# Kernel tuning notes

Hardware: AMD Instinct MI355X
Metric: run time of the kernel (lower is better)

## Reference

```python
import jax, jax.numpy as jnp
import numpy as np

H = 1024      # hidden_size
I = 4096      # intermediate_size (4*H SwiGLU)
E = 8         # num_experts
TOPK = 2      # num_experts_per_tok


def setup_inputs() -> dict:
    key = jax.random.key(0)
    ks = jax.random.split(key, 6)
    B, S = 4, 2048
    hidden_states = jax.random.normal(ks[0], (B, S, H), dtype=jnp.float32)
    # router gate (no bias)
    gate_w = jax.random.normal(ks[1], (H, E), dtype=jnp.float32) * (1.0 / np.sqrt(H))
    # per-expert SwiGLU weights (xavier-ish scale)
    W1 = jax.random.normal(ks[2], (E, H, I), dtype=jnp.float32) * np.sqrt(2.0 / (H + I))
    W3 = jax.random.normal(ks[3], (E, H, I), dtype=jnp.float32) * np.sqrt(2.0 / (H + I))
    W2 = jax.random.normal(ks[4], (E, I, H), dtype=jnp.float32) * np.sqrt(2.0 / (H + I))
    # per-expert domain embedding (added to expert input), init std 0.02
    dom = jax.random.normal(ks[5], (E, H), dtype=jnp.float32) * 0.02
    return {"hidden_states": hidden_states, "gate_w": gate_w,
            "W1": W1, "W2": W2, "W3": W3, "dom": dom}


def reference(hidden_states, gate_w, W1, W2, W3, dom):
    B, S, Hd = hidden_states.shape
    x = hidden_states.reshape(-1, Hd)                      # [T, H]
    router_logits = x @ gate_w                             # [T, E]
    top_logits, top_idx = jax.lax.top_k(router_logits, TOPK)
    weights = jax.nn.softmax(top_logits, axis=-1)          # [T, K]
    # dense per-(token, expert) combine weight; 0 for unselected experts
    w_dense = jnp.einsum('tk,tke->te', weights,
                         jax.nn.one_hot(top_idx, E, dtype=weights.dtype))  # [T, E]
    out = jnp.zeros_like(x)
    for e in range(E):  # small fixed expert loop (structurally distinct weights)
        xe = x + dom[e]                                    # domain embedding add
        h = jax.nn.silu(xe @ W1[e]) * (xe @ W3[e])         # SwiGLU [T, I]
        out = out + w_dense[:, e:e + 1] * (h @ W2[e])      # weighted combine
    return out.reshape(B, S, Hd)
```

## Files before the change

kernel.cpp:

```cpp
#include <hip/hip_runtime.h>
#include <hip/hip_bf16.h>
#include <stdint.h>

#define T_TOK 8192
#define H_DIM 1024
#define I_DIM 4096
#define NEXP  8
#define BM    128
#define FBK   64
#define RT_TILES 136
#define RMAX (RT_TILES * BM)

typedef __attribute__((ext_vector_type(8))) short bf16x8;
typedef __attribute__((ext_vector_type(4))) float f32x4;

__device__ __forceinline__ unsigned short f2bf(float f) {
    unsigned int u = __float_as_uint(f);
    return (unsigned short)((u + 0x7FFFu + ((u >> 16) & 1u)) >> 16);
}
__device__ __forceinline__ unsigned int pk2(float a, float b) {
    return (unsigned int)f2bf(a) | ((unsigned int)f2bf(b) << 16);
}
__device__ __forceinline__ void gl_lds16(const void* g, void* l) {
    __builtin_amdgcn_global_load_lds(
        (const __attribute__((address_space(1))) unsigned int*)g,
        (__attribute__((address_space(3))) unsigned int*)l, 16, 0, 0);
}

__global__ __launch_bounds__(256) void router_k(const float* __restrict__ x,
                                                const float* __restrict__ gw,
                                                int2* __restrict__ ridx,
                                                float2* __restrict__ rw) {
    __shared__ float gwT[NEXP][H_DIM + 8];
    for (int i = threadIdx.x; i < H_DIM * NEXP; i += 256) {
        const int k = i >> 3, e = i & 7;
        gwT[e][k] = gw[i];
    }
    __syncthreads();
    const int wid = threadIdx.x >> 6, lane = threadIdx.x & 63;
    const int t = blockIdx.x * 4 + wid;
    const float4* xr = (const float4*)(x + (size_t)t * H_DIM);
    float acc[NEXP];
#pragma unroll
    for (int e = 0; e < NEXP; ++e) acc[e] = 0.f;
#pragma unroll
    for (int jj = 0; jj < 4; ++jj) {
        const float4 v = xr[jj * 64 + lane];
        const int kb = jj * 256 + lane * 4;
#pragma unroll
        for (int e = 0; e < NEXP; ++e) {
            const float4 g = *(const float4*)&gwT[e][kb];
            acc[e] += v.x * g.x + v.y * g.y + v.z * g.z + v.w * g.w;
        }
    }
#pragma unroll
    for (int e = 0; e < NEXP; ++e) {
#pragma unroll
        for (int off = 32; off > 0; off >>= 1) acc[e] += __shfl_xor(acc[e], off, 64);
    }
    if (lane == 0) {
        int i0 = 0; float l0 = acc[0];
#pragma unroll
        for (int e = 1; e < NEXP; ++e) if (acc[e] > l0) { l0 = acc[e]; i0 = e; }
        int i1 = -1; float l1 = -3.4e38f;
#pragma unroll
        for (int e = 0; e < NEXP; ++e) if (e != i0 && acc[e] > l1) { l1 = acc[e]; i1 = e; }
        float ee = __expf(l1 - l0);
        float w0 = 1.f / (1.f + ee);
        float w1 = 1.f - w0;
        ridx[t] = make_int2(i0, i1);
        rw[t]   = make_float2(w0, w1);
    }
}

__global__ __launch_bounds__(256) void plan_k(const int2* __restrict__ ridx,
                                              int* __restrict__ offs,
                                              int* __restrict__ rpos) {
    __shared__ int cnt[256][NEXP];
    __shared__ int base_sh[256][NEXP];
    __shared__ int tot_sh[NEXP];
    __shared__ int offs_sh[NEXP + 1];
    const int tid = threadIdx.x;
    const int t0 = tid * (T_TOK / 256);
    int c[NEXP];
#pragma unroll
    for (int e = 0; e < NEXP; ++e) c[e] = 0;
    for (int j = 0; j < T_TOK / 256; ++j) {
        const int2 ii = ridx[t0 + j];
#pragma unroll
        for (int e = 0; e < NEXP; ++e)
            c[e] += (ii.x == e ? 1 : 0) + (ii.y == e ? 1 : 0);
    }
#pragma unroll
    for (int e = 0; e < NEXP; ++e) cnt[tid][e] = c[e];
    __syncthreads();
    if (tid < NEXP) {
        int s = 0;
        for (int i = 0; i < 256; ++i) s += cnt[i][tid];
        tot_sh[tid] = s;
    }
    __syncthreads();
    if (tid == 0) {
        int o = 0;
#pragma unroll
        for (int e = 0; e < NEXP; ++e) {
            offs_sh[e] = o; offs[e] = o;
            o += (tot_sh[e] + BM - 1) & ~(BM - 1);
        }
        offs_sh[NEXP] = o; offs[NEXP] = o;
    }
    __syncthreads();
    if (tid < NEXP) {
        int run = offs_sh[tid];
        for (int i = 0; i < 256; ++i) {
            base_sh[i][tid] = run;
            run += cnt[i][tid];
        }
    }
    __syncthreads();
    int b[NEXP];
#pragma unroll
    for (int e = 0; e < NEXP; ++e) b[e] = base_sh[tid][e];
    for (int j = 0; j < T_TOK / 256; ++j) {
        const int2 ii = ridx[t0 + j];
        int r0 = 0, r1 = 0;
#pragma unroll
        for (int e = 0; e < NEXP; ++e) r0 += (ii.x == e ? b[e] : 0);
#pragma unroll
        for (int e = 0; e < NEXP; ++e) b[e] += (ii.x == e ? 1 : 0);
#pragma unroll
        for (int e = 0; e < NEXP; ++e) r1 += (ii.y == e ? b[e] : 0);
#pragma unroll
        for (int e = 0; e < NEXP; ++e) b[e] += (ii.y == e ? 1 : 0);
        rpos[2 * (t0 + j)]     = r0;
        rpos[2 * (t0 + j) + 1] = r1;
    }
}

__global__ __launch_bounds__(256) void scatter_w13t_k(
        const float* __restrict__ x, const float* __restrict__ dom,
        const int2* __restrict__ ridx, const float2* __restrict__ rw,
        const int* __restrict__ rpos, float* __restrict__ rwgt,
        unsigned short* __restrict__ xg,
        const float* __restrict__ W1, const float* __restrict__ W3,
        unsigned short* __restrict__ w13) {
    __shared__ float st[64 * 65];
    if (blockIdx.x < 2048) {
        const int wid = threadIdx.x >> 6, lane = threadIdx.x & 63;
        const int t = blockIdx.x * 4 + wid;
        const int2 ii = ridx[t];
        const float2 ww = rw[t];
        const int r0 = rpos[2 * t], r1 = rpos[2 * t + 1];
        if (lane == 0) {
            rwgt[r0] = ww.x;
            rwgt[r1] = ww.y;
        }
        const float4* xr = (const float4*)(x + (size_t)t * H_DIM);
        float4 xv[4];
#pragma unroll
        for (int jj = 0; jj < 4; ++jj) xv[jj] = xr[jj * 64 + lane];
#pragma unroll
        for (int s = 0; s < 2; ++s) {
            const int e = s ? ii.y : ii.x;
            const int rr = s ? r1 : r0;
            const float4* dr = (const float4*)(dom + (size_t)e * H_DIM);
            unsigned short* op = xg + (size_t)rr * H_DIM;
#pragma unroll
            for (int jj = 0; jj < 4; ++jj) {
                const float4 b = dr[jj * 64 + lane];
                const int kb = jj * 256 + lane * 4;
                *(uint2*)(op + kb) = make_uint2(pk2(xv[jj].x + b.x, xv[jj].y + b.y),
                                                pk2(xv[jj].z + b.z, xv[jj].w + b.w));
            }
        }
    } else {
        const int idx = blockIdx.x - 2048;
        const int nt = idx & 63;
        const int kt = (idx >> 6) & 15;
        const int z  = idx >> 10;
        const int e = z >> 1, sel = z & 1;
        const float* src = (sel ? W3 : W1) + (size_t)e * H_DIM * I_DIM;
        const int t = threadIdx.x;
        const int kr = t >> 2, c0 = (t & 3) << 4;
        const float* sp = src + (size_t)(kt * 64 + kr) * I_DIM + nt * 64 + c0;
#pragma unroll
        for (int j = 0; j < 4; ++j) {
            float4 v = *(const float4*)(sp + j * 4);
            st[kr * 65 + c0 + j*4 + 0] = v.x; st[kr * 65 + c0 + j*4 + 1] = v.y;
            st[kr * 65 + c0 + j*4 + 2] = v.z; st[kr * 65 + c0 + j*4 + 3] = v.w;
        }
        __syncthreads();
        const int nl = t >> 2, k0 = (t & 3) << 4;
        const int n = nt * 64 + nl;
        const size_t drow = (size_t)e * 8192 + (size_t)((n >> 4) << 5) + (sel << 4) + (n & 15);
        unsigned short* dp = w13 + drow * H_DIM + kt * 64 + k0;
        unsigned int pk[8];
#pragma unroll
        for (int j = 0; j < 8; ++j)
            pk[j] = pk2(st[(k0 + 2*j) * 65 + nl], st[(k0 + 2*j + 1) * 65 + nl]);
        *(uint4*)dp = make_uint4(pk[0], pk[1], pk[2], pk[3]);
        *(uint4*)(dp + 8) = make_uint4(pk[4], pk[5], pk[6], pk[7]);
    }
}

__global__ __launch_bounds__(256, 3) void gemm1_w2t_k(
        const unsigned short* __restrict__ xg,
        const unsigned short* __restrict__ w13,
        const int* __restrict__ offs,
        unsigned short* __restrict__ h,
        const float* __restrict__ W2,
        unsigned short* __restrict__ w2t) {
    __shared__ unsigned short smem[2 * BM * FBK];
    if (blockIdx.x < 8704) {
        unsigned short* As = smem;
        unsigned short* Bs = smem + BM * FBK;
        const int wg = blockIdx.x;
        const int bx = wg & 63, by = wg >> 6;
        const int r0 = by * BM;
        if (r0 >= offs[NEXP]) return;
        int e = 0;
#pragma unroll
        for (int i = 1; i < NEXP; ++i) if (offs[i] <= r0) e = i;

        const int t = threadIdx.x, wid = t >> 6, lane = t & 63;
        const int srow = wid * 8 + (lane >> 3);
        const int schunk = (lane & 7) ^ (lane >> 3);
        const unsigned short* Agp = xg + (size_t)(r0 + srow) * H_DIM + (schunk << 3);
        const unsigned short* Bgp = w13 + ((size_t)e * 8192 + bx * 128 + srow) * H_DIM + (schunk << 3);
        unsigned short* Al = As + wid * 512;
        unsigned short* Bl = Bs + wid * 512;

        const int fr = lane & 15, g = lane >> 4, h3 = lane & 7;
        const int wr = (wid >> 1) * 64, wc = (wid & 1) * 64;

        f32x4 acc[4][4];
#pragma unroll
        for (int m = 0; m < 4; ++m)
#pragma unroll
            for (int n = 0; n < 4; ++n) acc[m][n] = (f32x4){0.f, 0.f, 0.f, 0.f};

#pragma unroll 1
        for (int kt = 0; kt < H_DIM / FBK; ++kt) {
            __syncthreads();
#pragma unroll
            for (int i = 0; i < 4; ++i) {
                gl_lds16(Agp + kt * FBK + i * 32 * H_DIM, Al + i * 2048);
                gl_lds16(Bgp + kt * FBK + i * 32 * H_DIM, Bl + i * 2048);
            }
            __syncthreads();
#pragma unroll
            for (int s = 0; s < 2; ++s) {
                const int pc = (((s << 2) + g) ^ h3) << 3;
                bf16x8 a[4], b[4];
#pragma unroll
                for (int m = 0; m < 4; ++m)
                    a[m] = *(const bf16x8*)&As[(wr + m * 16 + fr) * FBK + pc];
#pragma unroll
                for (int n = 0; n < 4; ++n)
                    b[n] = *(const bf16x8*)&Bs[(wc + n * 16 + fr) * FBK + pc];
#pragma unroll
                for (int m = 0; m < 4; ++m)
#pragma unroll
                    for (int n = 0; n < 4; ++n)
                        acc[m][n] = __builtin_amdgcn_mfma_f32_16x16x32_bf16(a[m], b[n], acc[m][n], 0, 0, 0);
            }
        }
        const int colbase = bx * 64 + ((wc >> 5) << 4) + fr;
#pragma unroll
        for (int m = 0; m < 4; ++m) {
            const int rbase = r0 + wr + m * 16 + (g << 2);
#pragma unroll
            for (int q = 0; q < 4; ++q) {
                unsigned short* hp = h + (size_t)(rbase + q) * I_DIM;
#pragma unroll
                for (int p = 0; p < 2; ++p) {
                    float p1 = acc[m][2 * p][q], p3 = acc[m][2 * p + 1][q];
                    float sv = p1 / (1.f + __expf(-p1));
                    hp[colbase + p * 16] = f2bf(sv * p3);
                }
            }
        }
    } else {
        float* st = (float*)smem;
        const int idx = blockIdx.x - 8704;
        const int nt = idx & 15;
        const int kt = (idx >> 4) & 63;
        const int e  = idx >> 10;
        const float* src = W2 + (size_t)e * I_DIM * H_DIM;
        const int t = threadIdx.x;
        const int kr = t >> 2, c0 = (t & 3) << 4;
        const float* sp = src + (size_t)(kt * 64 + kr) * H_DIM + nt * 64 + c0;
#pragma unroll
        for (int j = 0; j < 4; ++j) {
            float4 v = *(const float4*)(sp + j * 4);
            st[kr * 65 + c0 + j*4 + 0] = v.x; st[kr * 65 + c0 + j*4 + 1] = v.y;
            st[kr * 65 + c0 + j*4 + 2] = v.z; st[kr * 65 + c0 + j*4 + 3] = v.w;
        }
        __syncthreads();
        const int nl = t >> 2, k0 = (t & 3) << 4;
        unsigned short* dp = w2t + ((size_t)e * 1024 + nt * 64 + nl) * I_DIM + kt * 64 + k0;
        unsigned int pk[8];
#pragma unroll
        for (int j = 0; j < 8; ++j)
            pk[j] = pk2(st[(k0 + 2*j) * 65 + nl], st[(k0 + 2*j + 1) * 65 + nl]);
        *(uint4*)dp = make_uint4(pk[0], pk[1], pk[2], pk[3]);
        *(uint4*)(dp + 8) = make_uint4(pk[4], pk[5], pk[6], pk[7]);
    }
}

__global__ __launch_bounds__(256, 3) void gemm2_ksplit_k(
        const unsigned short* __restrict__ hbuf,
        const unsigned short* __restrict__ w2t,
        const int* __restrict__ offs,
        float* __restrict__ y) {
    __shared__ unsigned short As[BM * FBK];
    __shared__ unsigned short Bs[BM * FBK];
    const int bid = blockIdx.x;
    const int ks = (bid >= 1088) ? 1 : 0;
    const int sb = bid - ks * 1088;
    const int idx = sb >> 3;
    const int by = (sb & 7) * 17 + (idx >> 3);
    const int bx = idx & 7;
    const int r0 = by * BM;
    if (r0 >= offs[NEXP]) return;
    int e = 0;
#pragma unroll
    for (int i = 1; i < NEXP; ++i) if (offs[i] <= r0) e = i;

    const int t = threadIdx.x, wid = t >> 6, lane = t & 63;
    const int srow = wid * 8 + (lane >> 3);
    const int schunk = (lane & 7) ^ (lane >> 3);
    const unsigned short* Agp = hbuf + (size_t)(r0 + srow) * I_DIM + (schunk << 3);
    const unsigned short* Bgp = w2t + ((size_t)e * 1024 + bx * 128 + srow) * I_DIM + (schunk << 3);
    unsigned short* Al = &As[wid * 512];
    unsigned short* Bl = &Bs[wid * 512];

    const int fr = lane & 15, g = lane >> 4, h3 = lane & 7;
    const int wr = (wid >> 1) * 64, wc = (wid & 1) * 64;

    f32x4 acc[4][4];
#pragma unroll
    for (int m = 0; m < 4; ++m)
#pragma unroll
        for (int n = 0; n < 4; ++n) acc[m][n] = (f32x4){0.f, 0.f, 0.f, 0.f};

    const int kt0 = ks * 32;
#pragma unroll 1
    for (int kt = kt0; kt < kt0 + 32; ++kt) {
        __syncthreads();
#pragma unroll
        for (int i = 0; i < 4; ++i) {
            gl_lds16(Agp + kt * FBK + (size_t)i * 32 * I_DIM, Al + i * 2048);
            gl_lds16(Bgp + kt * FBK + (size_t)i * 32 * I_DIM, Bl + i * 2048);
        }
        __syncthreads();
#pragma unroll
        for (int s = 0; s < 2; ++s) {
            const int pcc = (((s << 2) + g) ^ h3) << 3;
            bf16x8 av[4], bv[4];
#pragma unroll
            for (int m = 0; m < 4; ++m)
                av[m] = *(const bf16x8*)&As[(wr + m * 16 + fr) * FBK + pcc];
#pragma unroll
            for (int n = 0; n < 4; ++n)
                bv[n] = *(const bf16x8*)&Bs[(wc + n * 16 + fr) * FBK + pcc];
#pragma unroll
            for (int m = 0; m < 4; ++m)
#pragma unroll
                for (int n = 0; n < 4; ++n)
                    acc[m][n] = __builtin_amdgcn_mfma_f32_16x16x32_bf16(av[m], bv[n], acc[m][n], 0, 0, 0);
        }
    }
    float* yo = y + (size_t)ks * ((size_t)RMAX * H_DIM);
#pragma unroll
    for (int m = 0; m < 4; ++m) {
#pragma unroll
        for (int q = 0; q < 4; ++q) {
            const int rr = r0 + wr + m * 16 + (g << 2) + q;
            float* yp = yo + (size_t)rr * H_DIM + bx * 128 + wc + fr;
#pragma unroll
            for (int n = 0; n < 4; ++n) yp[n * 16] = acc[m][n][q];
        }
    }
}

__global__ __launch_bounds__(256) void combine_k(const float* __restrict__ y,
                                                 const int* __restrict__ rpos,
                                                 const float* __restrict__ rwgt,
                                                 float* __restrict__ out) {
    const float* y1 = y + (size_t)RMAX * H_DIM;
    const int wid = threadIdx.x >> 6, lane = threadIdx.x & 63;
    const int t = blockIdx.x * 4 + wid;
    const int ra = rpos[2 * t], rb = rpos[2 * t + 1];
    const float wa = rwgt[ra], wb = rwgt[rb];
    const float4* pa0 = (const float4*)(y  + (size_t)ra * H_DIM);
    const float4* pa1 = (const float4*)(y1 + (size_t)ra * H_DIM);
    const float4* pb0 = (const float4*)(y  + (size_t)rb * H_DIM);
    const float4* pb1 = (const float4*)(y1 + (size_t)rb * H_DIM);
    float4* po = (float4*)(out + (size_t)t * H_DIM);
#pragma unroll
    for (int j = 0; j < 4; ++j) {
        const int i = lane + j * 64;
        float4 a0 = pa0[i], a1 = pa1[i], b0 = pb0[i], b1 = pb1[i];
        po[i] = make_float4(wa * (a0.x + a1.x) + wb * (b0.x + b1.x),
                            wa * (a0.y + a1.y) + wb * (b0.y + b1.y),
                            wa * (a0.z + a1.z) + wb * (b0.z + b1.z),
                            wa * (a0.w + a1.w) + wb * (b0.w + b1.w));
    }
}

#define WS_OFFS  0
#define WS_RIDX  256
#define WS_RW    (WS_RIDX + T_TOK * 8)
#define WS_RWGT  (WS_RW + T_TOK * 8)
#define WS_RPOS  (WS_RWGT + RMAX * 4)
#define WS_W13   266752
#define WS_XG    (WS_W13 + (size_t)134217728)
#define WS_W2T   (WS_XG + (size_t)RMAX * H_DIM * 2)
#define WS_H     (WS_W2T + (size_t)67108864)
#define WS_Y     WS_W13

extern "C" void kernel_launch(void* const* d_in, const int* in_sizes, int n_in,
                              void* d_out, int out_size, void* d_ws, size_t ws_size,
                              hipStream_t stream) {
    (void)in_sizes; (void)n_in; (void)ws_size; (void)out_size;
    const float* x   = (const float*)d_in[0];
    const float* gw  = (const float*)d_in[1];
    const float* W1  = (const float*)d_in[2];
    const float* W2  = (const float*)d_in[3];
    const float* W3  = (const float*)d_in[4];
    const float* dom = (const float*)d_in[5];
    float* out = (float*)d_out;

    char* ws = (char*)d_ws;
    int*    offs   = (int*)(ws + WS_OFFS);
    int2*   ridx   = (int2*)(ws + WS_RIDX);
    float2* rw     = (float2*)(ws + WS_RW);
    float*  rwgt   = (float*)(ws + WS_RWGT);
    int*    rpos   = (int*)(ws + WS_RPOS);
    unsigned short* w13 = (unsigned short*)(ws + WS_W13);
    unsigned short* xg  = (unsigned short*)(ws + WS_XG);
    unsigned short* w2t = (unsigned short*)(ws + WS_W2T);
    unsigned short* hb  = (unsigned short*)(ws + WS_H);
    float*          y   = (float*)(ws + WS_Y);

    router_k<<<T_TOK / 4, 256, 0, stream>>>(x, gw, ridx, rw);
    plan_k<<<1, 256, 0, stream>>>(ridx, offs, rpos);
    scatter_w13t_k<<<2048 + 16384, 256, 0, stream>>>(x, dom, ridx, rw, rpos, rwgt, xg,
                                                     W1, W3, w13);
    gemm1_w2t_k<<<8704 + 8192, 256, 0, stream>>>(xg, w13, offs, hb, W2, w2t);
    gemm2_ksplit_k<<<2176, 256, 0, stream>>>(hb, w2t, offs, y);
    combine_k<<<T_TOK / 4, 256, 0, stream>>>(y, rpos, rwgt, out);
}
```

Measured before the change: 608.3 us.

## Rewrite gemm2 as 256x128-tile triple-buffered pipelined kernel with per-expert tile table

Result: slower. 624.1 us (+2.6%).

```diff
diff --git a/kernel.cpp b/kernel.cpp
--- a/kernel.cpp
+++ b/kernel.cpp
@@ -10,6 +10,8 @@
 #define FBK   64
 #define RT_TILES 136
 #define RMAX (RT_TILES * BM)
+#define NTILE_MAX 72
+#define NKT 32
 
 typedef __attribute__((ext_vector_type(8))) short bf16x8;
 typedef __attribute__((ext_vector_type(4))) float f32x4;
@@ -75,7 +77,8 @@
 
 __global__ __launch_bounds__(256) void plan_k(const int2* __restrict__ ridx,
                                               int* __restrict__ offs,
-                                              int* __restrict__ rpos) {
+                                              int* __restrict__ rpos,
+                                              int* __restrict__ tinfo) {
     __shared__ int cnt[256][NEXP];
     __shared__ int base_sh[256][NEXP];
     __shared__ int tot_sh[NEXP];
@@ -108,6 +111,17 @@
             o += (tot_sh[e] + BM - 1) & ~(BM - 1);
         }
         offs_sh[NEXP] = o; offs[NEXP] = o;
+        int ntl = 0;
+        for (int e2 = 0; e2 < NEXP; ++e2) {
+            const int oe = offs_sh[e2], on = offs_sh[e2 + 1];
+            for (int r = oe; r < on; r += 256) {
+                tinfo[1 + ntl] = r;
+                tinfo[1 + NTILE_MAX + ntl] = e2;
+                tinfo[1 + 2 * NTILE_MAX + ntl] = (r + 256 < on) ? r + 256 : on;
+                ++ntl;
+            }
+        }
+        tinfo[0] = ntl;
     }
     __syncthreads();
     if (tid < NEXP) {
@@ -308,78 +322,114 @@
     }
 }
 
-__global__ __launch_bounds__(256, 3) void gemm2_ksplit_k(
+#define STG_A3(kt_, bf_) do { \
+    gl_lds16(pA0 + (size_t)(kt_) * 64, L + (bf_) * 16384 + 0 * 4096 + dof); \
+    gl_lds16(pA1 + (size_t)(kt_) * 64, L + (bf_) * 16384 + 1 * 4096 + dof); \
+    gl_lds16(pA2 + (size_t)(kt_) * 64, L + (bf_) * 16384 + 2 * 4096 + dof); } while (0)
+#define STG_A1B2(kt_, bf_) do { \
+    gl_lds16(pA3 + (size_t)(kt_) * 64, L + (bf_) * 16384 + 3 * 4096 + dof); \
+    gl_lds16(pB0 + (size_t)(kt_) * 64, LB + (bf_) * 8192 + 0 * 4096 + dof); \
+    gl_lds16(pB1 + (size_t)(kt_) * 64, LB + (bf_) * 8192 + 1 * 4096 + dof); } while (0)
+#define LDAB(s_, bf_) do { const int pc = ((((s_) << 2) + g) ^ h3) << 3; \
+    _Pragma("unroll") for (int m = 0; m < 4; ++m) \
+        a[m] = *(const bf16x8*)(Ard + (bf_) * 16384 + m * 1024 + pc); \
+    _Pragma("unroll") for (int n = 0; n < 4; ++n) \
+        b[n] = *(const bf16x8*)(Brd + (bf_) * 8192 + n * 1024 + pc); } while (0)
+#define MM16 do { __builtin_amdgcn_s_setprio(1); \
+    _Pragma("unroll") for (int m = 0; m < 4; ++m) \
+    _Pragma("unroll") for (int n = 0; n < 4; ++n) \
+        acc[m][n] = __builtin_amdgcn_mfma_f32_16x16x32_bf16(a[m], b[n], acc[m][n], 0, 0, 0); \
+    __builtin_amdgcn_s_setprio(0); } while (0)
+
+__global__ __launch_bounds__(512, 2) void gemm2_8ph_k(
         const unsigned short* __restrict__ hbuf,
         const unsigned short* __restrict__ w2t,
-        const int* __restrict__ offs,
+        const int* __restrict__ tinfo,
         float* __restrict__ y) {
-    __shared__ unsigned short As[BM * FBK];
-    __shared__ unsigned short Bs[BM * FBK];
+    __shared__ unsigned short L[3 * 16384 + 3 * 8192];
     const int bid = blockIdx.x;
-    const int ks = (bid >= 1088) ? 1 : 0;
-    const int sb = bid - ks * 1088;
+    const int ks = (bid >= 576) ? 1 : 0;
+    const int sb = bid - ks * 576;
     const int idx = sb >> 3;
-    const int by = (sb & 7) * 17 + (idx >> 3);
+    const int by = (sb & 7) * 9 + (idx >> 3);
     const int bx = idx & 7;
-    const int r0 = by * BM;
-    if (r0 >= offs[NEXP]) return;
-    int e = 0;
-#pragma unroll
-    for (int i = 1; i < NEXP; ++i) if (offs[i] <= r0) e = i;
-
-    const int t = threadIdx.x, wid = t >> 6, lane = t & 63;
-    const int srow = wid * 8 + (lane >> 3);
-    const int schunk = (lane & 7) ^ (lane >> 3);
-    const unsigned short* Agp = hbuf + (size_t)(r0 + srow) * I_DIM + (schunk << 3);
-    const unsigned short* Bgp = w2t + ((size_t)e * 1024 + bx * 128 + srow) * I_DIM + (schunk << 3);
-    unsigned short* Al = &As[wid * 512];
-    unsigned short* Bl = &Bs[wid * 512];
-
+    if (by >= tinfo[0]) return;
+    const int r0   = tinfo[1 + by];
+    const int e    = tinfo[1 + NTILE_MAX + by];
+    const int rend = tinfo[1 + 2 * NTILE_MAX + by];
+
+    const int t = threadIdx.x;
+    const int wid = t >> 6, lane = t & 63;
+    const int wm = wid >> 1, wn = wid & 1;
     const int fr = lane & 15, g = lane >> 4, h3 = lane & 7;
-    const int wr = (wid >> 1) * 64, wc = (wid & 1) * 64;
+
+    const int grow = t >> 3;
+    const int gcx  = (t & 7) ^ (grow & 7);
+    const size_t kbase = (size_t)ks * 2048 + (size_t)gcx * 8;
+    int ra0 = r0 + 0 * 64 + grow;  if (ra0 > RMAX - 1) ra0 = RMAX - 1;
+    int ra1 = r0 + 1 * 64 + grow;  if (ra1 > RMAX - 1) ra1 = RMAX - 1;
+    int ra2 = r0 + 2 * 64 + grow;  if (ra2 > RMAX - 1) ra2 = RMAX - 1;
+    int ra3 = r0 + 3 * 64 + grow;  if (ra3 > RMAX - 1) ra3 = RMAX - 1;
+    const unsigned short* pA0 = hbuf + (size_t)ra0 * I_DIM + kbase;
+    const unsigned short* pA1 = hbuf + (size_t)ra1 * I_DIM + kbase;
+    const unsigned short* pA2 = hbuf + (size_t)ra2 * I_DIM + kbase;
+    const unsigned short* pA3 = hbuf + (size_t)ra3 * I_DIM + kbase;
+    const unsigned short* pB0 = w2t + ((size_t)e * 1024 + bx * 128 + 0 * 64 + grow) * I_DIM + kbase;
+    const unsigned short* pB1 = w2t + ((size_t)e * 1024 + bx * 128 + 1 * 64 + grow) * I_DIM + kbase;
+    unsigned short* LB = L + 3 * 16384;
+    const int dof = t * 8;
+
+    const unsigned short* Ard = L  + (wm * 64 + fr) * 64;
+    const unsigned short* Brd = LB + (wn * 64 + fr) * 64;
 
     f32x4 acc[4][4];
 #pragma unroll
     for (int m = 0; m < 4; ++m)
 #pragma unroll
         for (int n = 0; n < 4; ++n) acc[m][n] = (f32x4){0.f, 0.f, 0.f, 0.f};
-
-    const int kt0 = ks * 32;
+    bf16x8 a[4], b[4];
+
+    STG_A3(0, 0); STG_A1B2(0, 0);
+    STG_A3(1, 1); STG_A1B2(1, 1);
+    asm volatile("s_waitcnt vmcnt(6)" ::: "memory");
+    __builtin_amdgcn_s_barrier();
+
+    int bc = 0, bs = 2;
 #pragma unroll 1
-    for (int kt = kt0; kt < kt0 + 32; ++kt) {
-        __syncthreads();
-#pragma unroll
-        for (int i = 0; i < 4; ++i) {
-            gl_lds16(Agp + kt * FBK + (size_t)i * 32 * I_DIM, Al + i * 2048);
-            gl_lds16(Bgp + kt * FBK + (size_t)i * 32 * I_DIM, Bl + i * 2048);
-        }
-        __syncthreads();
-#pragma unroll
-        for (int s = 0; s < 2; ++s) {
-            const int pcc = (((s << 2) + g) ^ h3) << 3;
-            bf16x8 av[4], bv[4];
-#pragma unroll
-            for (int m = 0; m < 4; ++m)
-                av[m] = *(const bf16x8*)&As[(wr + m * 16 + fr) * FBK + pcc];
-#pragma unroll
-            for (int n = 0; n < 4; ++n)
-                bv[n] = *(const bf16x8*)&Bs[(wc + n * 16 + fr) * FBK + pcc];
-#pragma unroll
-            for (int m = 0; m < 4; ++m)
-#pragma unroll
-                for (int n = 0; n < 4; ++n)
-                    acc[m][n] = __builtin_amdgcn_mfma_f32_16x16x32_bf16(av[m], bv[n], acc[m][n], 0, 0, 0);
-        }
-    }
+    for (int kt = 0; kt < NKT; ++kt) {
+        const int st = (kt < NKT - 2);
+        LDAB(0, bc);
+        if (st) STG_A3(kt + 2, bs);
+        __builtin_amdgcn_s_barrier();
+        MM16;
+        __builtin_amdgcn_s_barrier();
+        LDAB(1, bc);
+        if (st) {
+            STG_A1B2(kt + 2, bs);
+            asm volatile("s_waitcnt vmcnt(6)" ::: "memory");
+        } else if (kt == NKT - 2) {
+            asm volatile("s_waitcnt vmcnt(0)" ::: "memory");
+        }
+        __builtin_amdgcn_s_barrier();
+        MM16;
+        __builtin_amdgcn_s_barrier();
+        bc = (bc == 2) ? 0 : bc + 1;
+        bs = (bs == 2) ? 0 : bs + 1;
+    }
+
     float* yo = y + (size_t)ks * ((size_t)RMAX * H_DIM);
+    const int colb = bx * 128 + wn * 64 + fr;
 #pragma unroll
     for (int m = 0; m < 4; ++m) {
+        const int rb = r0 + wm * 64 + m * 16 + (g << 2);
 #pragma unroll
         for (int q = 0; q < 4; ++q) {
-            const int rr = r0 + wr + m * 16 + (g << 2) + q;
-            float* yp = yo + (size_t)rr * H_DIM + bx * 128 + wc + fr;
-#pragma unroll
-            for (int n = 0; n < 4; ++n) yp[n * 16] = acc[m][n][q];
+            const int rr = rb + q;
+            if (rr < rend) {
+                float* yp = yo + (size_t)rr * H_DIM + colb;
+#pragma unroll
+                for (int n = 0; n < 4; ++n) yp[n * 16] = acc[m][n][q];
+            }
         }
     }
 }
@@ -410,11 +460,12 @@
 }
 
 #define WS_OFFS  0
-#define WS_RIDX  256
+#define WS_TILE  256
+#define WS_RIDX  1280
 #define WS_RW    (WS_RIDX + T_TOK * 8)
 #define WS_RWGT  (WS_RW + T_TOK * 8)
 #define WS_RPOS  (WS_RWGT + RMAX * 4)
-#define WS_W13   266752
+#define WS_W13   267520
 #define WS_XG    (WS_W13 + (size_t)134217728)
 #define WS_W2T   (WS_XG + (size_t)RMAX * H_DIM * 2)
 #define WS_H     (WS_W2T + (size_t)67108864)
@@ -434,6 +485,7 @@
 
     char* ws = (char*)d_ws;
     int*    offs   = (int*)(ws + WS_OFFS);
+    int*    tinfo  = (int*)(ws + WS_TILE);
     int2*   ridx   = (int2*)(ws + WS_RIDX);
     float2* rw     = (float2*)(ws + WS_RW);
     float*  rwgt   = (float*)(ws + WS_RWGT);
@@ -445,10 +497,10 @@
     float*          y   = (float*)(ws + WS_Y);
 
     router_k<<<T_TOK / 4, 256, 0, stream>>>(x, gw, ridx, rw);
-    plan_k<<<1, 256, 0, stream>>>(ridx, offs, rpos);
+    plan_k<<<1, 256, 0, stream>>>(ridx, offs, rpos, tinfo);
     scatter_w13t_k<<<2048 + 16384, 256, 0, stream>>>(x, dom, ridx, rw, rpos, rwgt, xg,
                                                      W1, W3, w13);
     gemm1_w2t_k<<<8704 + 8192, 256, 0, stream>>>(xg, w13, offs, hb, W2, w2t);
-    gemm2_ksplit_k<<<2176, 256, 0, stream>>>(hb, w2t, offs, y);
+    gemm2_8ph_k<<<1152, 512, 0, stream>>>(hb, w2t, tinfo, y);
     combine_k<<<T_TOK / 4, 256, 0, stream>>>(y, rpos, rwgt, out);
 }
```

## Rewrite gemm1 as 256x256-tile 8-wave double-buffered kernel with tile table

Applied to the files above, without the earlier changes.

Measured after the change: 693.4 us. +14.0%, slower.

```diff
diff --git a/kernel.cpp b/kernel.cpp
--- a/kernel.cpp
+++ b/kernel.cpp
@@ -10,6 +10,7 @@
 #define FBK   64
 #define RT_TILES 136
 #define RMAX (RT_TILES * BM)
+#define NTILE_MAX 72
 
 typedef __attribute__((ext_vector_type(8))) short bf16x8;
 typedef __attribute__((ext_vector_type(4))) float f32x4;
@@ -75,7 +76,8 @@
 
 __global__ __launch_bounds__(256) void plan_k(const int2* __restrict__ ridx,
                                               int* __restrict__ offs,
-                                              int* __restrict__ rpos) {
+                                              int* __restrict__ rpos,
+                                              int* __restrict__ tinfo) {
     __shared__ int cnt[256][NEXP];
     __shared__ int base_sh[256][NEXP];
     __shared__ int tot_sh[NEXP];
@@ -108,6 +110,17 @@
             o += (tot_sh[e] + BM - 1) & ~(BM - 1);
         }
         offs_sh[NEXP] = o; offs[NEXP] = o;
+        int ntl = 0;
+        for (int e2 = 0; e2 < NEXP; ++e2) {
+            const int oe = offs_sh[e2], on = offs_sh[e2 + 1];
+            for (int r = oe; r < on; r += 256) {
+                tinfo[1 + ntl] = r;
+                tinfo[1 + NTILE_MAX + ntl] = e2;
+                tinfo[1 + 2 * NTILE_MAX + ntl] = (r + 256 < on) ? r + 256 : on;
+                ++ntl;
+            }
+        }
+        tinfo[0] = ntl;
     }
     __syncthreads();
     if (tid < NEXP) {
@@ -203,92 +216,132 @@
     }
 }
 
-__global__ __launch_bounds__(256, 3) void gemm1_w2t_k(
+#define SBAR __builtin_amdgcn_s_barrier()
+
+#define STG(kt_, b_) do { const size_t ko = (size_t)(kt_) * 64; \
+    gl_lds16(pA0 + ko, L + (b_) * 16384 + 0 * 4096 + dof); \
+    gl_lds16(pA1 + ko, L + (b_) * 16384 + 1 * 4096 + dof); \
+    gl_lds16(pA2 + ko, L + (b_) * 16384 + 2 * 4096 + dof); \
+    gl_lds16(pA3 + ko, L + (b_) * 16384 + 3 * 4096 + dof); \
+    gl_lds16(pB0 + ko, L + 32768 + (b_) * 16384 + 0 * 4096 + dof); \
+    gl_lds16(pB1 + ko, L + 32768 + (b_) * 16384 + 1 * 4096 + dof); \
+    gl_lds16(pB2 + ko, L + 32768 + (b_) * 16384 + 2 * 4096 + dof); \
+    gl_lds16(pB3 + ko, L + 32768 + (b_) * 16384 + 3 * 4096 + dof); } while (0)
+
+#define LDA(mh_, b_) do { _Pragma("unroll") for (int mi = 0; mi < 4; ++mi) { \
+    a[mi][0] = *(const bf16x8*)(Ard + (b_) * 16384 + ((mh_) * 64 + mi * 16) * 64 + cb0); \
+    a[mi][1] = *(const bf16x8*)(Ard + (b_) * 16384 + ((mh_) * 64 + mi * 16) * 64 + cb1); } } while (0)
+
+#define LDB(nh_, dst, b_) do { _Pragma("unroll") for (int ni = 0; ni < 2; ++ni) { \
+    dst[ni][0] = *(const bf16x8*)(Brd + (b_) * 16384 + ((nh_) * 2 + ni) * 1024 + cb0); \
+    dst[ni][1] = *(const bf16x8*)(Brd + (b_) * 16384 + ((nh_) * 2 + ni) * 1024 + cb1); } } while (0)
+
+#define MMQ(mh_, nh_, bb) do { __builtin_amdgcn_s_setprio(1); \
+    _Pragma("unroll") for (int mi = 0; mi < 4; ++mi) \
+    _Pragma("unroll") for (int ni = 0; ni < 2; ++ni) { \
+        acc[(mh_) * 4 + mi][(nh_) * 2 + ni] = __builtin_amdgcn_mfma_f32_16x16x32_bf16( \
+            a[mi][0], bb[ni][0], acc[(mh_) * 4 + mi][(nh_) * 2 + ni], 0, 0, 0); \
+        acc[(mh_) * 4 + mi][(nh_) * 2 + ni] = __builtin_amdgcn_mfma_f32_16x16x32_bf16( \
+            a[mi][1], bb[ni][1], acc[(mh_) * 4 + mi][(nh_) * 2 + ni], 0, 0, 0); } \
+    __builtin_amdgcn_s_setprio(0); } while (0)
+
+__global__ __launch_bounds__(512, 2) void gemm1_8ph_k(
         const unsigned short* __restrict__ xg,
         const unsigned short* __restrict__ w13,
-        const int* __restrict__ offs,
+        const int* __restrict__ tinfo,
         unsigned short* __restrict__ h,
         const float* __restrict__ W2,
         unsigned short* __restrict__ w2t) {
-    __shared__ unsigned short smem[2 * BM * FBK];
-    if (blockIdx.x < 8704) {
-        unsigned short* As = smem;
-        unsigned short* Bs = smem + BM * FBK;
-        const int wg = blockIdx.x;
-        const int bx = wg & 63, by = wg >> 6;
-        const int r0 = by * BM;
-        if (r0 >= offs[NEXP]) return;
-        int e = 0;
-#pragma unroll
-        for (int i = 1; i < NEXP; ++i) if (offs[i] <= r0) e = i;
-
-        const int t = threadIdx.x, wid = t >> 6, lane = t & 63;
-        const int srow = wid * 8 + (lane >> 3);
-        const int schunk = (lane & 7) ^ (lane >> 3);
-        const unsigned short* Agp = xg + (size_t)(r0 + srow) * H_DIM + (schunk << 3);
-        const unsigned short* Bgp = w13 + ((size_t)e * 8192 + bx * 128 + srow) * H_DIM + (schunk << 3);
-        unsigned short* Al = As + wid * 512;
-        unsigned short* Bl = Bs + wid * 512;
-
-        const int fr = lane & 15, g = lane >> 4, h3 = lane & 7;
-        const int wr = (wid >> 1) * 64, wc = (wid & 1) * 64;
-
-        f32x4 acc[4][4];
-#pragma unroll
-        for (int m = 0; m < 4; ++m)
+    __shared__ unsigned short L[65536];
+    const int bid = blockIdx.x;
+    if (bid < 2304) {
+        const int by = bid >> 5, bx = bid & 31;
+        if (by >= tinfo[0]) return;
+        const int r0   = tinfo[1 + by];
+        const int e    = tinfo[1 + NTILE_MAX + by];
+        const int rend = tinfo[1 + 2 * NTILE_MAX + by];
+
+        const int t = threadIdx.x;
+        const int wid = t >> 6, lane = t & 63;
+        const int wm = wid >> 2, wn = wid & 3;
+        const int fr = lane & 15, g = lane >> 4, h3 = fr & 7;
+
+        const int srow = t >> 3;
+        const int csrc = (t & 7) ^ (srow & 7);
+        int ra0 = r0 + 0 * 64 + srow; if (ra0 > RMAX - 1) ra0 = RMAX - 1;
+        int ra1 = r0 + 1 * 64 + srow; if (ra1 > RMAX - 1) ra1 = RMAX - 1;
+        int ra2 = r0 + 2 * 64 + srow; if (ra2 > RMAX - 1) ra2 = RMAX - 1;
+        int ra3 = r0 + 3 * 64 + srow; if (ra3 > RMAX - 1) ra3 = RMAX - 1;
+        const unsigned short* pA0 = xg + (size_t)ra0 * H_DIM + csrc * 8;
+        const unsigned short* pA1 = xg + (size_t)ra1 * H_DIM + csrc * 8;
+        const unsigned short* pA2 = xg + (size_t)ra2 * H_DIM + csrc * 8;
+        const unsigned short* pA3 = xg + (size_t)ra3 * H_DIM + csrc * 8;
+        const size_t brow = (size_t)e * 8192 + (size_t)bx * 256 + srow;
+        const unsigned short* pB0 = w13 + (brow + 0 * 64) * H_DIM + csrc * 8;
+        const unsigned short* pB1 = w13 + (brow + 1 * 64) * H_DIM + csrc * 8;
+        const unsigned short* pB2 = w13 + (brow + 2 * 64) * H_DIM + csrc * 8;
+        const unsigned short* pB3 = w13 + (brow + 3 * 64) * H_DIM + csrc * 8;
+        const int dof = wid * 512;
+
+        const int cb0 = ((0 + g) ^ h3) << 3;
+        const int cb1 = ((4 + g) ^ h3) << 3;
+        const unsigned short* Ard = L + (wm * 128 + fr) * 64;
+        const unsigned short* Brd = L + 32768 + (wn * 64 + fr) * 64;
+
+        f32x4 acc[8][4];
+#pragma unroll
+        for (int m = 0; m < 8; ++m)
 #pragma unroll
             for (int n = 0; n < 4; ++n) acc[m][n] = (f32x4){0.f, 0.f, 0.f, 0.f};
+        bf16x8 a[4][2], b0[2][2], b1[2][2];
+
+        STG(0, 0); STG(1, 1);
+        asm volatile("s_waitcnt vmcnt(8)" ::: "memory");
+        SBAR;
 
 #pragma unroll 1
-        for (int kt = 0; kt < H_DIM / FBK; ++kt) {
-            __syncthreads();
-#pragma unroll
-            for (int i = 0; i < 4; ++i) {
-                gl_lds16(Agp + kt * FBK + i * 32 * H_DIM, Al + i * 2048);
-                gl_lds16(Bgp + kt * FBK + i * 32 * H_DIM, Bl + i * 2048);
-            }
-            __syncthreads();
-#pragma unroll
-            for (int s = 0; s < 2; ++s) {
-                const int pc = (((s << 2) + g) ^ h3) << 3;
-                bf16x8 a[4], b[4];
-#pragma unroll
-                for (int m = 0; m < 4; ++m)
-                    a[m] = *(const bf16x8*)&As[(wr + m * 16 + fr) * FBK + pc];
-#pragma unroll
-                for (int n = 0; n < 4; ++n)
-                    b[n] = *(const bf16x8*)&Bs[(wc + n * 16 + fr) * FBK + pc];
-#pragma unroll
-                for (int m = 0; m < 4; ++m)
-#pragma unroll
-                    for (int n = 0; n < 4; ++n)
-                        acc[m][n] = __builtin_amdgcn_mfma_f32_16x16x32_bf16(a[m], b[n], acc[m][n], 0, 0, 0);
-            }
-        }
-        const int colbase = bx * 64 + ((wc >> 5) << 4) + fr;
-#pragma unroll
-        for (int m = 0; m < 4; ++m) {
-            const int rbase = r0 + wr + m * 16 + (g << 2);
+        for (int kt = 0; kt < 16; ++kt) {
+            const int bc = kt & 1;
+            LDA(0, bc); LDB(0, b0, bc);
+            SBAR; MMQ(0, 0, b0); SBAR;
+            LDB(1, b1, bc);
+            SBAR; MMQ(0, 1, b1); SBAR;
+            LDA(1, bc);
+            SBAR; MMQ(1, 1, b1); SBAR;
+            if (kt < 14) STG(kt + 2, bc);
+            SBAR;
+            MMQ(1, 0, b0);
+            if (kt < 14)       asm volatile("s_waitcnt vmcnt(8)" ::: "memory");
+            else if (kt == 14) asm volatile("s_waitcnt vmcnt(0)" ::: "memory");
+            SBAR;
+        }
+
+#pragma unroll
+        for (int mq = 0; mq < 8; ++mq) {
+            const int rb = r0 + wm * 128 + mq * 16 + (g << 2);
 #pragma unroll
             for (int q = 0; q < 4; ++q) {
-                unsigned short* hp = h + (size_t)(rbase + q) * I_DIM;
-#pragma unroll
-                for (int p = 0; p < 2; ++p) {
-                    float p1 = acc[m][2 * p][q], p3 = acc[m][2 * p + 1][q];
-                    float sv = p1 / (1.f + __expf(-p1));
-                    hp[colbase + p * 16] = f2bf(sv * p3);
+                const int rr = rb + q;
+                if (rr < rend) {
+                    unsigned short* hp = h + (size_t)rr * I_DIM;
+#pragma unroll
+                    for (int p = 0; p < 2; ++p) {
+                        float p1 = acc[mq][2 * p][q], p3 = acc[mq][2 * p + 1][q];
+                        float sv = p1 / (1.f + __expf(-p1));
+                        hp[((bx * 8 + wn * 2 + p) << 4) + fr] = f2bf(sv * p3);
+                    }
                 }
             }
         }
     } else {
-        float* st = (float*)smem;
-        const int idx = blockIdx.x - 8704;
+        float* st = (float*)L + (threadIdx.x >> 8) * (64 * 65);
+        const int idx = (bid - 2304) * 2 + (threadIdx.x >> 8);
+        const int tt = threadIdx.x & 255;
         const int nt = idx & 15;
         const int kt = (idx >> 4) & 63;
         const int e  = idx >> 10;
         const float* src = W2 + (size_t)e * I_DIM * H_DIM;
-        const int t = threadIdx.x;
-        const int kr = t >> 2, c0 = (t & 3) << 4;
+        const int kr = tt >> 2, c0 = (tt & 3) << 4;
         const float* sp = src + (size_t)(kt * 64 + kr) * H_DIM + nt * 64 + c0;
 #pragma unroll
         for (int j = 0; j < 4; ++j) {
@@ -297,7 +350,7 @@
             st[kr * 65 + c0 + j*4 + 2] = v.z; st[kr * 65 + c0 + j*4 + 3] = v.w;
         }
         __syncthreads();
-        const int nl = t >> 2, k0 = (t & 3) << 4;
+        const int nl = tt >> 2, k0 = (tt & 3) << 4;
         unsigned short* dp = w2t + ((size_t)e * 1024 + nt * 64 + nl) * I_DIM + kt * 64 + k0;
         unsigned int pk[8];
 #pragma unroll
@@ -410,11 +463,12 @@
 }
 
 #define WS_OFFS  0
-#define WS_RIDX  256
+#define WS_TILE  256
+#define WS_RIDX  1280
 #define WS_RW    (WS_RIDX + T_TOK * 8)
 #define WS_RWGT  (WS_RW + T_TOK * 8)
 #define WS_RPOS  (WS_RWGT + RMAX * 4)
-#define WS_W13   266752
+#define WS_W13   267520
 #define WS_XG    (WS_W13 + (size_t)134217728)
 #define WS_W2T   (WS_XG + (size_t)RMAX * H_DIM * 2)
 #define WS_H     (WS_W2T + (size_t)67108864)
@@ -434,6 +488,7 @@
 
     char* ws = (char*)d_ws;
     int*    offs   = (int*)(ws + WS_OFFS);
+    int*    tinfo  = (int*)(ws + WS_TILE);
     int2*   ridx   = (int2*)(ws + WS_RIDX);
     float2* rw     = (float2*)(ws + WS_RW);
     float*  rwgt   = (float*)(ws + WS_RWGT);
@@ -445,10 +500,10 @@
     float*          y   = (float*)(ws + WS_Y);
 
     router_k<<<T_TOK / 4, 256, 0, stream>>>(x, gw, ridx, rw);
-    plan_k<<<1, 256, 0, stream>>>(ridx, offs, rpos);
+    plan_k<<<1, 256, 0, stream>>>(ridx, offs, rpos, tinfo);
     scatter_w13t_k<<<2048 + 16384, 256, 0, stream>>>(x, dom, ridx, rw, rpos, rwgt, xg,
                                                      W1, W3, w13);
-    gemm1_w2t_k<<<8704 + 8192, 256, 0, stream>>>(xg, w13, offs, hb, W2, w2t);
+    gemm1_8ph_k<<<2304 + 4096, 512, 0, stream>>>(xg, w13, tinfo, hb, W2, w2t);
     gemm2_ksplit_k<<<2176, 256, 0, stream>>>(hb, w2t, offs, y);
     combine_k<<<T_TOK / 4, 256, 0, stream>>>(y, rpos, rwgt, out);
 }
```
